# Optimization experiments

Hardware: AMD Instinct MI355X
Metric: run time of the kernel (lower is better)

The kernel has to match this reference:

```python
import jax, jax.numpy as jnp
import numpy as np

ALPHA, GAMMA = 0.25, 2.0
SPARSITY_PENALTY = 1.0
FOCAL_W, SPARSITY_W, CONC_W = 1.0, 0.8, 1.5
CONC_INNER_W = 1.0  # ConcentrationLoss(concentration_weight=1.0)


def setup_inputs() -> dict:
    key = jax.random.key(0)
    k1, k2 = jax.random.split(key)
    B, C, H, W = 16, 20, 256, 256
    pred = jax.random.normal(k1, (B, C, H, W), dtype=jnp.float32)
    target = (jax.random.uniform(k2, (B, C, H, W)) < 0.05).astype(jnp.float32)
    return {"pred": pred, "target": target}


def reference(pred, target):
    B, C, H, W = pred.shape
    p = jax.nn.sigmoid(pred)

    # ---- Focal loss ----
    is_pos = target == 1.0
    pt = jnp.where(is_pos, p, 1.0 - p)
    alpha_t = jnp.where(is_pos, ALPHA, 1.0 - ALPHA)
    focal = jnp.mean(-alpha_t * (1.0 - pt) ** GAMMA * jnp.log(pt + 1e-8))

    # ---- Sparsity loss ----
    sparsity = jnp.mean((pred - target) ** 2) + SPARSITY_PENALTY * jnp.mean(jnp.abs(pred))

    # ---- Concentration loss (vectorized over (b, c)) ----
    y = jnp.arange(H, dtype=jnp.float32)[:, None]   # [H,1]
    x = jnp.arange(W, dtype=jnp.float32)[None, :]   # [1,W]
    mass = target.sum(axis=(2, 3))                  # [B,C]
    valid = mass > 0
    safe_mass = jnp.where(valid, mass, 1.0)
    cy = jnp.einsum('bchw,hw->bc', target, jnp.broadcast_to(y, (H, W))) / safe_mass
    cx = jnp.einsum('bchw,hw->bc', target, jnp.broadcast_to(x, (H, W))) / safe_mass
    # squared distance to per-(b,c) target centroid: [B,C,H,W]
    dsq = (y[None, None] - cy[:, :, None, None]) ** 2 + (x[None, None] - cx[:, :, None, None]) ** 2
    per_sample = jnp.mean(p * dsq, axis=(2, 3))     # [B,C]
    n_valid = valid.sum()
    conc_sum = jnp.sum(jnp.where(valid, per_sample, 0.0))
    concentration = jnp.where(
        n_valid > 0,
        conc_sum / jnp.maximum(n_valid, 1).astype(jnp.float32),
        0.0,
    ) * CONC_INNER_W

    total = FOCAL_W * focal + SPARSITY_W * sparsity + CONC_W * concentration
    return total, focal, sparsity, concentration
```

## Files before the change

### kernel.cpp

```cpp
#include <hip/hip_runtime.h>
#include <math.h>

constexpr int Bn = 16, Cn = 20, Hn = 256, Wn = 256;
constexpr int BCn = Bn * Cn;
constexpr int HWn = Hn * Wn;
constexpr int SPLIT = 4;
constexpr int NBLK = BCn * SPLIT;
constexpr int CHUNK = HWn / SPLIT;
constexpr int TPB = 512;
constexpr int NWAVE = TPB / 64;
constexpr int V4 = CHUNK / (TPB * 4);
constexpr int NSLOT = 10;

__device__ inline float wave_reduce(float v) {
    #pragma unroll
    for (int o = 32; o > 0; o >>= 1) v += __shfl_down(v, o, 64);
    return v;
}

__global__ __launch_bounds__(TPB) void partials_kernel(
        const float* __restrict__ pred, const float* __restrict__ target,
        float* __restrict__ ws) {
    const int blk = blockIdx.x;
    const int bc = blk >> 2;
    const int chunk = blk & (SPLIT - 1);
    const long long base = (long long)bc * HWn + (long long)chunk * CHUNK;
    const float4* __restrict__ p4 = (const float4*)(pred + base);
    const float4* __restrict__ t4 = (const float4*)(target + base);
    const int tid = threadIdx.x;

    float st[4] = {0.f, 0.f, 0.f, 0.f};
    float sp[4] = {0.f, 0.f, 0.f, 0.f};
    float sty = 0.f, spy = 0.f, spyy = 0.f;
    float foc = 0.f, sq = 0.f, ab = 0.f;

    const int e_base = chunk * CHUNK + tid * 4;
    const float x0 = (float)(e_base & 255);
    float y = (float)(e_base >> 8);

    float4 pa = p4[tid];
    float4 ta = t4[tid];
    float4 pb = p4[TPB + tid];
    float4 tb = t4[TPB + tid];

    #pragma unroll
    for (int i = 0; i < V4; i++) {
        float4 pn, tn;
        if (i + 2 < V4) {
            pn = p4[(i + 2) * TPB + tid];
            tn = t4[(i + 2) * TPB + tid];
        }
        const float yy = y * y;
        const float pvals[4] = {pa.x, pa.y, pa.z, pa.w};
        const float tvals[4] = {ta.x, ta.y, ta.z, ta.w};
        float pj[4];
        #pragma unroll
        for (int j = 0; j < 4; j++) {
            const float v = pvals[j];
            const float t = tvals[j];
            const float e = __expf(-v);
            const float p = __builtin_amdgcn_rcpf(1.0f + e);
            pj[j] = p;
            const bool pos = (t > 0.5f);
            const float lp = __logf(p);
            const float lpt = pos ? lp : lp - v;
            const float q = pos ? fmaf(-0.5f, p, 0.5f) : 0.8660254f * p;
            foc = fmaf(q * q, lpt, foc);
            const float d = v - t;
            sq = fmaf(d, d, sq);
            ab += fabsf(v);
            st[j] += t;
            sp[j] += p;
        }
        const float s_t = (tvals[0] + tvals[1]) + (tvals[2] + tvals[3]);
        const float s_p = (pj[0] + pj[1]) + (pj[2] + pj[3]);
        sty  = fmaf(s_t, y,  sty);
        spy  = fmaf(s_p, y,  spy);
        spyy = fmaf(s_p, yy, spyy);
        y += 8.0f;
        pa = pb; ta = tb;
        if (i + 2 < V4) { pb = pn; tb = tn; }
    }

    const float x1 = x0 + 1.f, x2 = x0 + 2.f, x3 = x0 + 3.f;
    const float mass = (st[0] + st[1]) + (st[2] + st[3]);
    const float Sp   = (sp[0] + sp[1]) + (sp[2] + sp[3]);
    float stx  = x0 * st[0];
    stx = fmaf(x1, st[1], stx); stx = fmaf(x2, st[2], stx); stx = fmaf(x3, st[3], stx);
    float spx  = x0 * sp[0];
    spx = fmaf(x1, sp[1], spx); spx = fmaf(x2, sp[2], spx); spx = fmaf(x3, sp[3], spx);
    float spxx = (x0 * x0) * sp[0];
    spxx = fmaf(x1 * x1, sp[1], spxx);
    spxx = fmaf(x2 * x2, sp[2], spxx);
    spxx = fmaf(x3 * x3, sp[3], spxx);
    const float sprr = spyy + spxx;

    float acc[NSLOT] = {mass, sty, stx, Sp, spy, spx, sprr, foc, sq, ab};

    __shared__ float lds[NWAVE][NSLOT];
    const int lane = tid & 63, wave = tid >> 6;
    #pragma unroll
    for (int k = 0; k < NSLOT; k++) {
        const float r = wave_reduce(acc[k]);
        if (lane == 0) lds[wave][k] = r;
    }
    __syncthreads();
    if (tid < NSLOT) {
        float s = 0.f;
        #pragma unroll
        for (int w = 0; w < NWAVE; w++) s += lds[w][tid];
        ws[blk * NSLOT + tid] = s;
    }
}

__global__ __launch_bounds__(512) void finalize_kernel(
        const float* __restrict__ ws, float* __restrict__ out) {
    const int tid = threadIdx.x;

    float conc_sum = 0.f, nvalid = 0.f;
    if (tid < BCn) {
        float mass = 0, sty = 0, stx = 0, sp = 0, spy = 0, spx = 0, sprr = 0;
        for (int s = 0; s < SPLIT; s++) {
            const float* w = ws + (size_t)(tid * SPLIT + s) * NSLOT;
            mass += w[0]; sty += w[1]; stx += w[2]; sp += w[3];
            spy  += w[4]; spx += w[5]; sprr += w[6];
        }
        const bool valid = mass > 0.f;
        const float sm = valid ? mass : 1.0f;
        const float cy = sty / sm, cx = stx / sm;
        const float pdsq = sprr - 2.f * cy * spy - 2.f * cx * spx
                         + (cy * cy + cx * cx) * sp;
        conc_sum = valid ? (pdsq / (float)HWn) : 0.f;
        nvalid   = valid ? 1.f : 0.f;
    }

    float foc = 0.f, sq = 0.f, ab = 0.f;
    for (int blk = tid; blk < NBLK; blk += 512) {
        const float* w = ws + (size_t)blk * NSLOT;
        foc += w[7]; sq += w[8]; ab += w[9];
    }

    __shared__ float lds[8][5];
    const int lane = tid & 63, wave = tid >> 6;
    float vals[5] = {conc_sum, nvalid, foc, sq, ab};
    #pragma unroll
    for (int k = 0; k < 5; k++) {
        const float r = wave_reduce(vals[k]);
        if (lane == 0) lds[wave][k] = r;
    }
    __syncthreads();

    if (tid == 0) {
        float tot[5];
        #pragma unroll
        for (int k = 0; k < 5; k++) {
            float s = 0.f;
            #pragma unroll
            for (int w = 0; w < 8; w++) s += lds[w][k];
            tot[k] = s;
        }
        const float NTOT = (float)Bn * Cn * Hn * Wn;
        const float focal = -tot[2] / NTOT;
        const float sparsity = tot[3] / NTOT + tot[4] / NTOT;
        const float concentration =
            (tot[1] > 0.f) ? (tot[0] / fmaxf(tot[1], 1.f)) : 0.f;
        const float total = 1.0f * focal + 0.8f * sparsity + 1.5f * concentration;
        out[0] = total;
        out[1] = focal;
        out[2] = sparsity;
        out[3] = concentration;
    }
}

extern "C" void kernel_launch(void* const* d_in, const int* in_sizes, int n_in,
                              void* d_out, int out_size, void* d_ws, size_t ws_size,
                              hipStream_t stream) {
    const float* pred   = (const float*)d_in[0];
    const float* target = (const float*)d_in[1];
    float* out = (float*)d_out;
    float* ws  = (float*)d_ws;

    partials_kernel<<<NBLK, TPB, 0, stream>>>(pred, target, ws);
    finalize_kernel<<<1, 512, 0, stream>>>(ws, out);
}
```

Before: 191.8 us.

## Stream inputs via global_load_lds double-buffered LDS and halve block size

```diff
diff --git a/kernel.cpp b/kernel.cpp
--- a/kernel.cpp
+++ b/kernel.cpp
@@ -7,10 +7,13 @@
 constexpr int SPLIT = 4;
 constexpr int NBLK = BCn * SPLIT;
 constexpr int CHUNK = HWn / SPLIT;
-constexpr int TPB = 512;
+constexpr int TPB = 256;
 constexpr int NWAVE = TPB / 64;
 constexpr int V4 = CHUNK / (TPB * 4);
 constexpr int NSLOT = 10;
+
+#define GLOBAL_AS __attribute__((address_space(1)))
+#define LDS_AS    __attribute__((address_space(3)))
 
 __device__ inline float wave_reduce(float v) {
     #pragma unroll
@@ -18,9 +21,15 @@
     return v;
 }
 
+__device__ inline void dma16(const float4* g, float4* l) {
+    __builtin_amdgcn_global_load_lds((GLOBAL_AS const void*)g,
+                                     (LDS_AS void*)l, 16, 0, 0);
+}
+
 __global__ __launch_bounds__(TPB) void partials_kernel(
         const float* __restrict__ pred, const float* __restrict__ target,
         float* __restrict__ ws) {
+    __shared__ float4 sbuf[2][2][TPB];
     const int blk = blockIdx.x;
     const int bc = blk >> 2;
     const int chunk = blk & (SPLIT - 1);
@@ -28,28 +37,30 @@
     const float4* __restrict__ p4 = (const float4*)(pred + base);
     const float4* __restrict__ t4 = (const float4*)(target + base);
     const int tid = threadIdx.x;
+    const int wslot = (tid >> 6) << 6;
 
     float st[4] = {0.f, 0.f, 0.f, 0.f};
     float sp[4] = {0.f, 0.f, 0.f, 0.f};
     float sty = 0.f, spy = 0.f, spyy = 0.f;
     float foc = 0.f, sq = 0.f, ab = 0.f;
 
-    const int e_base = chunk * CHUNK + tid * 4;
-    const float x0 = (float)(e_base & 255);
-    float y = (float)(e_base >> 8);
+    const float x0 = (float)((tid & 63) << 2);
+    float y = (float)((chunk << 6) + (tid >> 6));
 
-    float4 pa = p4[tid];
-    float4 ta = t4[tid];
-    float4 pb = p4[TPB + tid];
-    float4 tb = t4[TPB + tid];
+    dma16(p4 + tid, &sbuf[0][0][wslot]);
+    dma16(t4 + tid, &sbuf[0][1][wslot]);
 
-    #pragma unroll
-    for (int i = 0; i < V4; i++) {
-        float4 pn, tn;
-        if (i + 2 < V4) {
-            pn = p4[(i + 2) * TPB + tid];
-            tn = t4[(i + 2) * TPB + tid];
+    for (int k = 0; k < V4; k++) {
+        const int buf = k & 1;
+        if (k + 1 < V4) {
+            dma16(p4 + (k + 1) * TPB + tid, &sbuf[buf ^ 1][0][wslot]);
+            dma16(t4 + (k + 1) * TPB + tid, &sbuf[buf ^ 1][1][wslot]);
         }
+        __syncthreads();
+        const float4 pa = sbuf[buf][0][tid];
+        const float4 ta = sbuf[buf][1][tid];
+        __syncthreads();
+
         const float yy = y * y;
         const float pvals[4] = {pa.x, pa.y, pa.z, pa.w};
         const float tvals[4] = {ta.x, ta.y, ta.z, ta.w};
@@ -77,9 +88,7 @@
         sty  = fmaf(s_t, y,  sty);
         spy  = fmaf(s_p, y,  spy);
         spyy = fmaf(s_p, yy, spyy);
-        y += 8.0f;
-        pa = pb; ta = tb;
-        if (i + 2 < V4) { pb = pn; tb = tn; }
+        y += 4.0f;
     }
 
     const float x1 = x0 + 1.f, x2 = x0 + 2.f, x3 = x0 + 3.f;
```

Result: no change. 192.6 us (+0.4%).
